# Kernel tuning notes

Measured on AMD Instinct MI355X. Metric: run time of the kernel, lower is better.

## Reference

```python
import jax, jax.numpy as jnp
import numpy as np

N, E = 50000, 800000
IN_C, H_C, OUT_C, HEADS = 64, 32, 32, 8


def setup_inputs() -> dict:
    key = jax.random.key(0)
    ks = jax.random.split(key, 16)
    def glorot(k, shape):
        fan_in = shape[-1]
        return jax.random.normal(k, shape, dtype=jnp.float32) / jnp.sqrt(jnp.float32(fan_in))
    inp = {
        'x': jax.random.normal(ks[0], (N, IN_C), dtype=jnp.float32),
        'edge_index': jax.random.randint(ks[1], (2, E), 0, N, dtype=jnp.int64),
        # layer 1: in_c -> h_c, heads
        'W1l': glorot(ks[2], (HEADS * H_C, IN_C)),
        'b1l': jnp.zeros((HEADS * H_C,), jnp.float32),
        'W1r': glorot(ks[3], (HEADS * H_C, IN_C)),
        'b1r': jnp.zeros((HEADS * H_C,), jnp.float32),
        'att1': glorot(ks[4], (HEADS, H_C)),
        'bias1': jnp.zeros((H_C,), jnp.float32),
        # layer 2: h_c -> out_c, heads
        'W2l': glorot(ks[5], (HEADS * OUT_C, H_C)),
        'b2l': jnp.zeros((HEADS * OUT_C,), jnp.float32),
        'W2r': glorot(ks[6], (HEADS * OUT_C, H_C)),
        'b2r': jnp.zeros((HEADS * OUT_C,), jnp.float32),
        'att2': glorot(ks[7], (HEADS, OUT_C)),
        'bias2': jnp.zeros((OUT_C,), jnp.float32),
    }
    return inp


def _gatv2_layer(x, src, dst, valid, Wl, bl, Wr, br, att, bias):
    # PyG GATv2Conv (share_weights=False, concat=False): message j->i uses
    # e = att . leaky_relu(lin_l(x_j) + lin_r(x_i), 0.2); softmax over dst; agg lin_l(x_j).
    n = x.shape[0]
    heads, c = att.shape
    xl = (x @ Wl.T + bl).reshape(n, heads, c)
    xr = (x @ Wr.T + br).reshape(n, heads, c)
    m = jax.nn.leaky_relu(xl[src] + xr[dst], negative_slope=0.2)  # [Etot,H,C]
    score = jnp.einsum('ehc,hc->eh', m, att)                      # [Etot,H]
    score = jnp.where(valid[:, None], score, -jnp.inf)
    smax = jax.ops.segment_max(score, dst, num_segments=n)        # [N,H]
    a = jnp.where(valid[:, None], jnp.exp(score - smax[dst]), 0.0)
    denom = jax.ops.segment_sum(a, dst, num_segments=n)
    a = a / jnp.maximum(denom[dst], 1e-16)
    out = jax.ops.segment_sum(a[..., None] * xl[src], dst, num_segments=n)  # [N,H,C]
    return out.mean(axis=1) + bias


def reference(x, edge_index, W1l, b1l, W1r, b1r, att1, bias1,
              W2l, b2l, W2r, b2r, att2, bias2):
    n = x.shape[0]
    src0, dst0 = edge_index[0], edge_index[1]
    # PyG removes existing self loops then adds fresh ones: mask originals,
    # append one self loop per node (keeps static shapes).
    loop = jnp.arange(n, dtype=src0.dtype)
    src = jnp.concatenate([src0, loop])
    dst = jnp.concatenate([dst0, loop])
    valid = jnp.concatenate([src0 != dst0, jnp.ones((n,), bool)])
    h = _gatv2_layer(x, src, dst, valid, W1l, b1l, W1r, b1r, att1, bias1)
    h = jax.nn.leaky_relu(h, negative_slope=0.01)  # nn.LeakyReLU default
    out = _gatv2_layer(h, src, dst, valid, W2l, b2l, W2r, b2r, att2, bias2)
    return out
```

## Files before the change

### kernel.cpp

```cpp
#include <hip/hip_runtime.h>
#include <math.h>

#define HEADS 8
#define CDIM 32
#define ODIM 256
#define BKT_SHIFT 7
#define CHUNK 4096
#define CAP 4096
#define GB 512

typedef _Float16 h2 __attribute__((ext_vector_type(2)));
typedef _Float16 h4 __attribute__((ext_vector_type(4)));
typedef _Float16 h8 __attribute__((ext_vector_type(8)));
typedef float f32x4 __attribute__((ext_vector_type(4)));
typedef unsigned long long u64;
union H4 { h4 v; h2 p[2]; u64 u; };

#if __has_builtin(__builtin_amdgcn_fdot2)
#define FDOT2(a,b,c) __builtin_amdgcn_fdot2((a),(b),(c),false)
#else
static __device__ __forceinline__ float fdot2_sw(h2 a, h2 b, float c){
  return fmaf((float)a.x, (float)b.x, fmaf((float)a.y, (float)b.y, c));
}
#define FDOT2(a,b,c) fdot2_sw((a),(b),(c))
#endif

__device__ __forceinline__ float lrelu(float v, float s){ return fmaxf(v, s*v); }


__global__ __launch_bounds__(512) void csr_sort_kernel(
    const int* __restrict__ bpack, const int* __restrict__ btotal,
    int* __restrict__ csr, int* __restrict__ ind_beg, int* __restrict__ ind_end,
    int n, int B){
  __shared__ int lh[128], cur[128], ss[128];
  int b = blockIdx.x, t = threadIdx.x;
  int beg = b*CAP;
  int cnt = btotal[b]; if (cnt > CAP) cnt = CAP;
  if (t < 128) lh[t] = 0;
  __syncthreads();
  for (int j = t; j < cnt; j += 512)
    atomicAdd(&lh[bpack[beg+j] & 127], 1);
  __syncthreads();
  int v = (t < 128) ? lh[t] : 0;
  if (t < 128) ss[t] = v;
  __syncthreads();
  for (int off=1; off<128; off<<=1){
    int u = (t >= off && t < 128) ? ss[t-off] : 0;
    __syncthreads();
    if (t < 128) ss[t] += u;
    __syncthreads();
  }
  if (t < 128){
    int excl = ss[t] - v;
    cur[t] = excl;
    int node = (b << BKT_SHIFT) + t;
    if (node < n){ ind_beg[node] = beg + excl; ind_end[node] = beg + excl + v; }
  }
  __syncthreads();
  for (int j = t; j < cnt; j += 512){
    int p = bpack[beg + j];
    int lpos = atomicAdd(&cur[p & 127], 1);
    csr[beg + lpos] = p >> BKT_SHIFT;
  }
}

template<int K, bool FUSE_AUX, bool W_F32>
__global__ __launch_bounds__(512, 4) void gemm_mfma(const float* __restrict__ X,
    const void* __restrict__ Wl, const float* __restrict__ bl,
    const void* __restrict__ Wr, const float* __restrict__ br,
    _Float16* __restrict__ outl, _Float16* __restrict__ outr, int n,
    const int* __restrict__ src, const int* __restrict__ dst,
    int* __restrict__ bpack, int* __restrict__ bucket_cnt, int e, int B,
    const float* __restrict__ W2l, const float* __restrict__ W2r,
    _Float16* __restrict__ w2lh, _Float16* __restrict__ w2rh){
  if (FUSE_AUX && blockIdx.y == 1){
    int k = blockIdx.x;
    int NB = (e + CHUNK-1)/CHUNK;
    int t = threadIdx.x;
    if (k < NB){
      __shared__ int lh[512], bs[512];
      lh[t] = 0;
      __syncthreads();
      int base_i = k*CHUNK;
      int rr[CHUNK/512], dd[CHUNK/512], sv[CHUNK/512];
#pragma unroll
      for (int j = 0; j < CHUNK/512; ++j){
        int i = base_i + j*512 + t;
        rr[j] = -1; dd[j] = 0; sv[j] = 0;
        if (i < e){
          int s = src[i], d = dst[i];
          dd[j] = d; sv[j] = s;
          if (s != d) rr[j] = atomicAdd(&lh[d>>BKT_SHIFT], 1);
        }
      }
      __syncthreads();
      for (int b = t; b < B; b += 512)
        bs[b] = lh[b] ? atomicAdd(bucket_cnt + b, lh[b]) : 0;
      __syncthreads();
#pragma unroll
      for (int j = 0; j < CHUNK/512; ++j){
        if (rr[j] >= 0){
          int b = dd[j] >> BKT_SHIFT;
          bpack[b*CAP + bs[b] + rr[j]] = (sv[j] << BKT_SHIFT) | (dd[j] & 127);
        }
      }
    } else if (k < NB + 8){
      int i = ((k - NB)*512 + t)*4;
      const float* s; _Float16* d; int off;
      if (i < 8192){ s = W2l; d = w2lh; off = i; }
      else         { s = W2r; d = w2rh; off = i - 8192; }
      float4 v = *(const float4*)(s + off);
      *(h4*)(d + off) = (h4){(_Float16)v.x, (_Float16)v.y, (_Float16)v.z, (_Float16)v.w};
    }
    return;
  }
  const int KP = K + 8;
  const int NKS = K/32;
  const int NLD = (64*(K/4))/512;
  __shared__ __align__(16) _Float16 Xs[2][64*(K+8)];
  int t = threadIdx.x;
  int nt = (n + 63) >> 6;
  int tb0 = blockIdx.x;
  int tb1 = blockIdx.x + GB;
  bool has1 = (tb1 < nt);

#pragma unroll
  for (int j = 0; j < NLD; ++j){
    int idx = t + j*512;
    int row = idx/(K/4), c = (idx%(K/4))*4;
    int node = tb0*64 + row; if (node >= n) node = n-1;
    f32x4 xv = __builtin_nontemporal_load((const f32x4*)(X + (size_t)node*K + c));
    *(h4*)(Xs[0] + row*KP + c) = (h4){(_Float16)xv[0], (_Float16)xv[1],
                                      (_Float16)xv[2], (_Float16)xv[3]};
  }
  f32x4 p1[NLD];
  if (has1){
#pragma unroll
    for (int j = 0; j < NLD; ++j){
      int idx = t + j*512;
      int row = idx/(K/4), c = (idx%(K/4))*4;
      int node = tb1*64 + row; if (node >= n) node = n-1;
      p1[j] = __builtin_nontemporal_load((const f32x4*)(X + (size_t)node*K + c));
    }
  }
  __syncthreads();

  int wave = t >> 6, lane = t & 63;
  int co = wave*64;
  const void* W   = (co < 256) ? Wl : Wr;
  const float* Bv = (co < 256) ? bl : br;
  _Float16* outp  = (co < 256) ? outl : outr;
  int lco = co & 255;
  int lr = lane & 15, lg = lane >> 4;

  auto compute = [&](const _Float16* buf, int n0){
    f32x4 acc[4][4];
#pragma unroll
    for (int c = 0; c < 4; ++c)
#pragma unroll
      for (int m = 0; m < 4; ++m) acc[c][m] = (f32x4){0.f, 0.f, 0.f, 0.f};
#pragma unroll
    for (int ks = 0; ks < NKS; ++ks){
      int k0 = ks*32 + lg*8;
      h8 a[4], b[4];
#pragma unroll
      for (int c = 0; c < 4; ++c){
        if (W_F32){
          const float* wp = (const float*)W + (size_t)(lco + c*16 + lr)*K + k0;
          float4 w0 = *(const float4*)(wp);
          float4 w1 = *(const float4*)(wp + 4);
          a[c] = (h8){(_Float16)w0.x,(_Float16)w0.y,(_Float16)w0.z,(_Float16)w0.w,
                      (_Float16)w1.x,(_Float16)w1.y,(_Float16)w1.z,(_Float16)w1.w};
        } else {
          a[c] = *(const h8*)((const _Float16*)W + (size_t)(lco + c*16 + lr)*K + k0);
        }
      }
#pragma unroll
      for (int m = 0; m < 4; ++m)
        b[m] = *(const h8*)(buf + (m*16 + lr)*KP + k0);
#pragma unroll
      for (int c = 0; c < 4; ++c)
#pragma unroll
        for (int m = 0; m < 4; ++m)
          acc[c][m] = __builtin_amdgcn_mfma_f32_16x16x32_f16(a[c], b[m], acc[c][m], 0, 0, 0);
    }
#pragma unroll
    for (int c = 0; c < 4; ++c){
      int ch = lco + c*16 + lg*4;
      float4 bb = *(const float4*)(Bv + ch);
#pragma unroll
      for (int m = 0; m < 4; ++m){
        int node = n0 + m*16 + lr;
        if (node < n){
          h4 o = {(_Float16)(acc[c][m][0] + bb.x), (_Float16)(acc[c][m][1] + bb.y),
                  (_Float16)(acc[c][m][2] + bb.z), (_Float16)(acc[c][m][3] + bb.w)};
          *(h4*)(outp + (size_t)node*ODIM + ch) = o;
        }
      }
    }
  };

  compute(Xs[0], tb0*64);

  if (has1){
#pragma unroll
    for (int j = 0; j < NLD; ++j){
      int idx = t + j*512;
      int row = idx/(K/4), c = (idx%(K/4))*4;
      *(h4*)(Xs[1] + row*KP + c) = (h4){(_Float16)p1[j][0], (_Float16)p1[j][1],
                                        (_Float16)p1[j][2], (_Float16)p1[j][3]};
    }
    __syncthreads();
    compute(Xs[1], tb1*64);
  }
}

__global__ __launch_bounds__(256) void edge_kernel(
    const _Float16* __restrict__ xl, const _Float16* __restrict__ xr,
    const float* __restrict__ att, const float* __restrict__ bias,
    const int* __restrict__ ind_beg, const int* __restrict__ ind_end,
    const int* __restrict__ csr_src,
    float* __restrict__ out, int n, int act)
{
  int wid = blockIdx.x*4 + (threadIdx.x >> 6);
  if (wid >= n) return;
  int lane = threadIdx.x & 63;
  const float LOG2E = 1.44269504088896341f;

  float4 attf = *(const float4*)(att + 4*lane);
  h2 at0 = (h2){(_Float16)(attf.x*LOG2E), (_Float16)(attf.y*LOG2E)};
  h2 at1 = (h2){(_Float16)(attf.z*LOG2E), (_Float16)(attf.w*LOG2E)};
  const h2 c02 = {(_Float16)0.2f, (_Float16)0.2f};

  H4 xrh; xrh.u = __builtin_nontemporal_load((const u64*)(xr + (size_t)wid*ODIM + 4*lane));
  H4 self; self.v = *(const h4*)(xl + (size_t)wid*ODIM + 4*lane);

  auto score = [&](const H4& c)->float{
    h2 t0 = c.p[0] + xrh.p[0];
    h2 t1 = c.p[1] + xrh.p[1];
    h2 q0 = __builtin_elementwise_max(t0, t0 * c02);
    h2 q1 = __builtin_elementwise_max(t1, t1 * c02);
    float d = FDOT2(q0, at0, FDOT2(q1, at1, 0.f));
    d += __shfl_xor(d, 1);
    d += __shfl_xor(d, 2);
    d += __shfl_xor(d, 4);
    return d;
  };

  float w0 = exp2f(score(self));
  float denom = w0;
  float4 acc;
  acc.x = w0 * (float)self.v.x;
  acc.y = w0 * (float)self.v.y;
  acc.z = w0 * (float)self.v.z;
  acc.w = w0 * (float)self.v.w;

  int beg = __builtin_amdgcn_readfirstlane(ind_beg[wid]);
  int end = __builtin_amdgcn_readfirstlane(ind_end[wid]);
  int cnt = end - beg;

#define GATHER(j) (*(const h4*)(xl + (size_t)((unsigned)__shfl(sidx,(j)))*ODIM + 4*lane))
  for (int cb = 0; cb < cnt; cb += 64){
    int ccnt = min(cnt - cb, 64);
    int sidx = (lane < ccnt) ? __builtin_nontemporal_load(csr_src + beg + cb + lane) : 0;
    H4 r0, r1, r2, r3;
    r0.v = (h4){}; r1.v = (h4){}; r2.v = (h4){}; r3.v = (h4){};
    if (ccnt > 0) r0.v = GATHER(0);
    if (ccnt > 1) r1.v = GATHER(1);
    if (ccnt > 2) r2.v = GATHER(2);
    if (ccnt > 3) r3.v = GATHER(3);
#pragma unroll 2
    for (int k = 0; k < ccnt; k += 2){
      H4 e0 = r0, e1 = r1;
      r0 = r2; r1 = r3;
      if (k+4 < ccnt) r2.v = GATHER(k+4);
      if (k+5 < ccnt) r3.v = GATHER(k+5);
      float s0 = score(e0);
      float s1 = score(e1);
      float pe0 = exp2f(s0);
      float pe1 = (k+1 < ccnt) ? exp2f(s1) : 0.f;
      denom += pe0 + pe1;
      acc.x = fmaf(pe0, (float)e0.v.x, fmaf(pe1, (float)e1.v.x, acc.x));
      acc.y = fmaf(pe0, (float)e0.v.y, fmaf(pe1, (float)e1.v.y, acc.y));
      acc.z = fmaf(pe0, (float)e0.v.z, fmaf(pe1, (float)e1.v.z, acc.z));
      acc.w = fmaf(pe0, (float)e0.v.w, fmaf(pe1, (float)e1.v.w, acc.w));
    }
  }
#undef GATHER

  float inv = 1.f/denom;
  float vx = acc.x*inv, vy = acc.y*inv, vz = acc.z*inv, vw = acc.w*inv;
  vx += __shfl_xor(vx, 8);  vx += __shfl_xor(vx, 16);  vx += __shfl_xor(vx, 32);
  vy += __shfl_xor(vy, 8);  vy += __shfl_xor(vy, 16);  vy += __shfl_xor(vy, 32);
  vz += __shfl_xor(vz, 8);  vz += __shfl_xor(vz, 16);  vz += __shfl_xor(vz, 32);
  vw += __shfl_xor(vw, 8);  vw += __shfl_xor(vw, 16);  vw += __shfl_xor(vw, 32);
  if (lane < 8){
    float4 bv = *(const float4*)(bias + 4*lane);
    float ox = vx*0.125f + bv.x;
    float oy = vy*0.125f + bv.y;
    float oz = vz*0.125f + bv.z;
    float ow = vw*0.125f + bv.w;
    if (act){
      ox = lrelu(ox, 0.01f); oy = lrelu(oy, 0.01f);
      oz = lrelu(oz, 0.01f); ow = lrelu(ow, 0.01f);
    }
    f32x4 ov = {ox, oy, oz, ow};
    __builtin_nontemporal_store(ov, (f32x4*)(out + (size_t)wid*CDIM + 4*lane));
  }
}

extern "C" void kernel_launch(void* const* d_in, const int* in_sizes, int n_in,
                              void* d_out, int out_size, void* d_ws, size_t ws_size,
                              hipStream_t stream){
  (void)n_in; (void)out_size; (void)ws_size;
  const float* x    = (const float*)d_in[0];
  const int*   ei   = (const int*)d_in[1];
  const float* W1l  = (const float*)d_in[2];
  const float* b1l  = (const float*)d_in[3];
  const float* W1r  = (const float*)d_in[4];
  const float* b1r  = (const float*)d_in[5];
  const float* att1 = (const float*)d_in[6];
  const float* bias1= (const float*)d_in[7];
  const float* W2l  = (const float*)d_in[8];
  const float* b2l  = (const float*)d_in[9];
  const float* W2r  = (const float*)d_in[10];
  const float* b2r  = (const float*)d_in[11];
  const float* att2 = (const float*)d_in[12];
  const float* bias2= (const float*)d_in[13];
  int n = in_sizes[0] / 64;
  int e = in_sizes[1] / 2;
  const int* srcp = ei;
  const int* dstp = ei + e;

  char* ws = (char*)d_ws;
  size_t off = 0;
  auto alloc = [&](size_t bytes)->char*{
    char* p = ws + off; off += (bytes + 255) & ~(size_t)255; return p;
  };
  _Float16* xl  = (_Float16*)alloc((size_t)n*ODIM*2);
  _Float16* xr  = (_Float16*)alloc((size_t)n*ODIM*2);
  float* h      = (float*)alloc((size_t)n*CDIM*4);
  int*   ind_beg = (int*)alloc((size_t)n*4);
  int*   ind_end = (int*)alloc((size_t)n*4);

  int NB = (e + CHUNK-1) / CHUNK;
  int B  = (n + 127) >> 7;
  int*   csr    = (int*)alloc((size_t)B*CAP*4);
  int*   bpack  = (int*)alloc((size_t)B*CAP*4);
  int*   bucket_cnt = (int*)alloc((size_t)B*4);
  _Float16* w2lh = (_Float16*)alloc((size_t)ODIM*32*2);
  _Float16* w2rh = (_Float16*)alloc((size_t)ODIM*32*2);

  hipMemsetAsync(bucket_cnt, 0, (size_t)B*4, stream);
  gemm_mfma<64,true,true><<<dim3(GB,2), 512, 0, stream>>>(
      x, W1l, b1l, W1r, b1r, xl, xr, n, srcp, dstp, bpack, bucket_cnt, e, B,
      W2l, W2r, w2lh, w2rh);
  csr_sort_kernel<<<B, 512, 0, stream>>>(bpack, bucket_cnt, csr, ind_beg, ind_end, n, B);

  edge_kernel<<<(n+3)/4, 256, 0, stream>>>(xl, xr, att1, bias1, ind_beg, ind_end, csr, h, n, 1);
  gemm_mfma<32,false,false><<<dim3(GB,1), 512, 0, stream>>>(
      h, w2lh, b2l, w2rh, b2r, xl, xr, n, nullptr, nullptr, nullptr, nullptr, 0, 0,
      nullptr, nullptr, nullptr, nullptr);
  edge_kernel<<<(n+3)/4, 256, 0, stream>>>(xl, xr, att2, bias2, ind_beg, ind_end, csr, (float*)d_out, n, 0);
}
```

Baseline: 294.9 us.

## Split GEMM across output halves with 256-thread blocks, drop two-tile prefetch

The GEMM now launches one 64-node tile per block with 256 threads and uses blockIdx.y to pick the left or right projection half. This replaces 512-thread blocks that each handled two node tiles with a software-prefetched second tile. The auxiliary edge-bucketing and weight-conversion work moves to y=2 and is adapted to 256 threads. The goal is more blocks and better occupancy and load balance. In exchange, each node tile of X is loaded and converted twice (once per half), and the manual prefetch overlap is lost.

```diff
diff --git a/kernel.cpp b/kernel.cpp
--- a/kernel.cpp
+++ b/kernel.cpp
@@ -7,7 +7,6 @@
 #define BKT_SHIFT 7
 #define CHUNK 4096
 #define CAP 4096
-#define GB 512
 
 typedef _Float16 h2 __attribute__((ext_vector_type(2)));
 typedef _Float16 h4 __attribute__((ext_vector_type(4)));
@@ -65,7 +64,7 @@
 }
 
 template<int K, bool FUSE_AUX, bool W_F32>
-__global__ __launch_bounds__(512, 4) void gemm_mfma(const float* __restrict__ X,
+__global__ __launch_bounds__(256) void gemm_mfma(const float* __restrict__ X,
     const void* __restrict__ Wl, const float* __restrict__ bl,
     const void* __restrict__ Wr, const float* __restrict__ br,
     _Float16* __restrict__ outl, _Float16* __restrict__ outr, int n,
@@ -73,19 +72,19 @@
     int* __restrict__ bpack, int* __restrict__ bucket_cnt, int e, int B,
     const float* __restrict__ W2l, const float* __restrict__ W2r,
     _Float16* __restrict__ w2lh, _Float16* __restrict__ w2rh){
-  if (FUSE_AUX && blockIdx.y == 1){
+  if (FUSE_AUX && blockIdx.y == 2){
     int k = blockIdx.x;
     int NB = (e + CHUNK-1)/CHUNK;
     int t = threadIdx.x;
     if (k < NB){
       __shared__ int lh[512], bs[512];
-      lh[t] = 0;
+      for (int b = t; b < 512; b += 256) lh[b] = 0;
       __syncthreads();
       int base_i = k*CHUNK;
-      int rr[CHUNK/512], dd[CHUNK/512], sv[CHUNK/512];
-#pragma unroll
-      for (int j = 0; j < CHUNK/512; ++j){
-        int i = base_i + j*512 + t;
+      int rr[CHUNK/256], dd[CHUNK/256], sv[CHUNK/256];
+#pragma unroll
+      for (int j = 0; j < CHUNK/256; ++j){
+        int i = base_i + j*256 + t;
         rr[j] = -1; dd[j] = 0; sv[j] = 0;
         if (i < e){
           int s = src[i], d = dst[i];
@@ -94,18 +93,18 @@
         }
       }
       __syncthreads();
-      for (int b = t; b < B; b += 512)
+      for (int b = t; b < B; b += 256)
         bs[b] = lh[b] ? atomicAdd(bucket_cnt + b, lh[b]) : 0;
       __syncthreads();
 #pragma unroll
-      for (int j = 0; j < CHUNK/512; ++j){
+      for (int j = 0; j < CHUNK/256; ++j){
         if (rr[j] >= 0){
           int b = dd[j] >> BKT_SHIFT;
           bpack[b*CAP + bs[b] + rr[j]] = (sv[j] << BKT_SHIFT) | (dd[j] & 127);
         }
       }
-    } else if (k < NB + 8){
-      int i = ((k - NB)*512 + t)*4;
+    } else if (k < NB + 16){
+      int i = ((k - NB)*256 + t)*4;
       const float* s; _Float16* d; int off;
       if (i < 8192){ s = W2l; d = w2lh; off = i; }
       else         { s = W2r; d = w2rh; off = i - 8192; }
@@ -116,102 +115,72 @@
   }
   const int KP = K + 8;
   const int NKS = K/32;
-  const int NLD = (64*(K/4))/512;
-  __shared__ __align__(16) _Float16 Xs[2][64*(K+8)];
+  __shared__ __align__(16) _Float16 Xs[64*(K+8)];
   int t = threadIdx.x;
-  int nt = (n + 63) >> 6;
-  int tb0 = blockIdx.x;
-  int tb1 = blockIdx.x + GB;
-  bool has1 = (tb1 < nt);
-
-#pragma unroll
-  for (int j = 0; j < NLD; ++j){
-    int idx = t + j*512;
+  int n0 = blockIdx.x*64;
+
+  for (int idx = t; idx < 64*(K/4); idx += 256){
     int row = idx/(K/4), c = (idx%(K/4))*4;
-    int node = tb0*64 + row; if (node >= n) node = n-1;
+    int node = n0 + row; if (node >= n) node = n-1;
     f32x4 xv = __builtin_nontemporal_load((const f32x4*)(X + (size_t)node*K + c));
-    *(h4*)(Xs[0] + row*KP + c) = (h4){(_Float16)xv[0], (_Float16)xv[1],
-                                      (_Float16)xv[2], (_Float16)xv[3]};
-  }
-  f32x4 p1[NLD];
-  if (has1){
-#pragma unroll
-    for (int j = 0; j < NLD; ++j){
-      int idx = t + j*512;
-      int row = idx/(K/4), c = (idx%(K/4))*4;
-      int node = tb1*64 + row; if (node >= n) node = n-1;
-      p1[j] = __builtin_nontemporal_load((const f32x4*)(X + (size_t)node*K + c));
-    }
+    *(h4*)(Xs + row*KP + c) = (h4){(_Float16)xv[0], (_Float16)xv[1],
+                                   (_Float16)xv[2], (_Float16)xv[3]};
   }
   __syncthreads();
 
   int wave = t >> 6, lane = t & 63;
-  int co = wave*64;
+  int co = blockIdx.y*256 + wave*64;
   const void* W   = (co < 256) ? Wl : Wr;
   const float* Bv = (co < 256) ? bl : br;
   _Float16* outp  = (co < 256) ? outl : outr;
   int lco = co & 255;
   int lr = lane & 15, lg = lane >> 4;
 
-  auto compute = [&](const _Float16* buf, int n0){
-    f32x4 acc[4][4];
+  f32x4 acc[4][4];
+#pragma unroll
+  for (int c = 0; c < 4; ++c)
+#pragma unroll
+    for (int m = 0; m < 4; ++m) acc[c][m] = (f32x4){0.f, 0.f, 0.f, 0.f};
+
+#pragma unroll
+  for (int ks = 0; ks < NKS; ++ks){
+    int k0 = ks*32 + lg*8;
+    h8 a[4], b[4];
+#pragma unroll
+    for (int c = 0; c < 4; ++c){
+      if (W_F32){
+        const float* wp = (const float*)W + (size_t)(lco + c*16 + lr)*K + k0;
+        float4 w0 = *(const float4*)(wp);
+        float4 w1 = *(const float4*)(wp + 4);
+        a[c] = (h8){(_Float16)w0.x,(_Float16)w0.y,(_Float16)w0.z,(_Float16)w0.w,
+                    (_Float16)w1.x,(_Float16)w1.y,(_Float16)w1.z,(_Float16)w1.w};
+      } else {
+        a[c] = *(const h8*)((const _Float16*)W + (size_t)(lco + c*16 + lr)*K + k0);
+      }
+    }
+#pragma unroll
+    for (int m = 0; m < 4; ++m)
+      b[m] = *(const h8*)(Xs + (m*16 + lr)*KP + k0);
 #pragma unroll
     for (int c = 0; c < 4; ++c)
 #pragma unroll
-      for (int m = 0; m < 4; ++m) acc[c][m] = (f32x4){0.f, 0.f, 0.f, 0.f};
-#pragma unroll
-    for (int ks = 0; ks < NKS; ++ks){
-      int k0 = ks*32 + lg*8;
-      h8 a[4], b[4];
-#pragma unroll
-      for (int c = 0; c < 4; ++c){
-        if (W_F32){
-          const float* wp = (const float*)W + (size_t)(lco + c*16 + lr)*K + k0;
-          float4 w0 = *(const float4*)(wp);
-          float4 w1 = *(const float4*)(wp + 4);
-          a[c] = (h8){(_Float16)w0.x,(_Float16)w0.y,(_Float16)w0.z,(_Float16)w0.w,
-                      (_Float16)w1.x,(_Float16)w1.y,(_Float16)w1.z,(_Float16)w1.w};
-        } else {
-          a[c] = *(const h8*)((const _Float16*)W + (size_t)(lco + c*16 + lr)*K + k0);
-        }
+      for (int m = 0; m < 4; ++m)
+        acc[c][m] = __builtin_amdgcn_mfma_f32_16x16x32_f16(a[c], b[m], acc[c][m], 0, 0, 0);
+  }
+
+#pragma unroll
+  for (int c = 0; c < 4; ++c){
+    int ch = lco + c*16 + lg*4;
+    float4 bb = *(const float4*)(Bv + ch);
+#pragma unroll
+    for (int m = 0; m < 4; ++m){
+      int node = n0 + m*16 + lr;
+      if (node < n){
+        h4 o = {(_Float16)(acc[c][m][0] + bb.x), (_Float16)(acc[c][m][1] + bb.y),
+                (_Float16)(acc[c][m][2] + bb.z), (_Float16)(acc[c][m][3] + bb.w)};
+        *(h4*)(outp + (size_t)node*ODIM + ch) = o;
       }
-#pragma unroll
-      for (int m = 0; m < 4; ++m)
-        b[m] = *(const h8*)(buf + (m*16 + lr)*KP + k0);
-#pragma unroll
-      for (int c = 0; c < 4; ++c)
-#pragma unroll
-        for (int m = 0; m < 4; ++m)
-          acc[c][m] = __builtin_amdgcn_mfma_f32_16x16x32_f16(a[c], b[m], acc[c][m], 0, 0, 0);
-    }
-#pragma unroll
-    for (int c = 0; c < 4; ++c){
-      int ch = lco + c*16 + lg*4;
-      float4 bb = *(const float4*)(Bv + ch);
-#pragma unroll
-      for (int m = 0; m < 4; ++m){
-        int node = n0 + m*16 + lr;
-        if (node < n){
-          h4 o = {(_Float16)(acc[c][m][0] + bb.x), (_Float16)(acc[c][m][1] + bb.y),
-                  (_Float16)(acc[c][m][2] + bb.z), (_Float16)(acc[c][m][3] + bb.w)};
-          *(h4*)(outp + (size_t)node*ODIM + ch) = o;
-        }
-      }
-    }
-  };
-
-  compute(Xs[0], tb0*64);
-
-  if (has1){
-#pragma unroll
-    for (int j = 0; j < NLD; ++j){
-      int idx = t + j*512;
-      int row = idx/(K/4), c = (idx%(K/4))*4;
-      *(h4*)(Xs[1] + row*KP + c) = (h4){(_Float16)p1[j][0], (_Float16)p1[j][1],
-                                        (_Float16)p1[j][2], (_Float16)p1[j][3]};
-    }
-    __syncthreads();
-    compute(Xs[1], tb1*64);
+    }
   }
 }
 
@@ -351,14 +320,16 @@
   _Float16* w2lh = (_Float16*)alloc((size_t)ODIM*32*2);
   _Float16* w2rh = (_Float16*)alloc((size_t)ODIM*32*2);
 
+  int nt64 = (n + 63) / 64;
+
   hipMemsetAsync(bucket_cnt, 0, (size_t)B*4, stream);
-  gemm_mfma<64,true,true><<<dim3(GB,2), 512, 0, stream>>>(
+  gemm_mfma<64,true,true><<<dim3(nt64,3), 256, 0, stream>>>(
       x, W1l, b1l, W1r, b1r, xl, xr, n, srcp, dstp, bpack, bucket_cnt, e, B,
       W2l, W2r, w2lh, w2rh);
   csr_sort_kernel<<<B, 512, 0, stream>>>(bpack, bucket_cnt, csr, ind_beg, ind_end, n, B);
 
   edge_kernel<<<(n+3)/4, 256, 0, stream>>>(xl, xr, att1, bias1, ind_beg, ind_end, csr, h, n, 1);
-  gemm_mfma<32,false,false><<<dim3(GB,1), 512, 0, stream>>>(
+  gemm_mfma<32,false,false><<<dim3(nt64,2), 256, 0, stream>>>(
       h, w2lh, b2l, w2rh, b2r, xl, xr, n, nullptr, nullptr, nullptr, nullptr, 0, 0,
       nullptr, nullptr, nullptr, nullptr);
   edge_kernel<<<(n+3)/4, 256, 0, stream>>>(xl, xr, att2, bias2, ind_beg, ind_end, csr, (float*)d_out, n, 0);
```

After: 307.6 us. 1.04x slower.
